# Performance work log

Measured on AMD Instinct MI355X. Metric: run time of the kernel, lower is better.

Reference implementation:

```python
import jax, jax.numpy as jnp
import numpy as np

K = 3          # per-row / per-col topk, from init kwarg k
THRESHOLD = 0.0


def setup_inputs() -> dict:
    key = jax.random.key(0)
    k1, k2 = jax.random.split(key)
    P, R, S = 512, 256, 256
    matching_score_map = jax.random.normal(k1, (P, R, S), dtype=jnp.float32)
    node_corr_scores = jax.random.uniform(k2, (P,), dtype=jnp.float32)
    ref_knn_masks = jnp.ones((P, R), dtype=bool)
    src_knn_masks = jnp.ones((P, S), dtype=bool)
    return {
        "matching_score_map": matching_score_map,
        "node_corr_scores": node_corr_scores,
        "ref_knn_masks": ref_knn_masks,
        "src_knn_masks": src_knn_masks,
    }


def reference(matching_score_map, node_corr_scores, ref_knn_masks, src_knn_masks):
    # score map: exp of log-matching scores  [P, R, S]
    score = jnp.exp(matching_score_map)
    P, R, S = score.shape
    # valid correspondence mask  [P, R, S]
    corr_mask = ref_knn_masks[:, :, None] & src_knn_masks[:, None, :]

    p_idx = jnp.arange(P)[:, None, None]

    # topk along src axis (dim=2), scatter back into a zero map
    ref_vals, ref_idx = jax.lax.top_k(score, K)                      # [P, R, K]
    ref_score_map = jnp.zeros_like(score).at[
        p_idx, jnp.arange(R)[None, :, None], ref_idx
    ].set(ref_vals)

    # topk along ref axis (dim=1): transpose so it is the last axis
    src_vals, src_idx = jax.lax.top_k(score.transpose(0, 2, 1), K)   # [P, S, K]
    src_score_map = jnp.zeros_like(score).at[
        p_idx, src_idx, jnp.arange(S)[None, :, None]
    ].set(src_vals)

    ref_corr_map = (ref_score_map > THRESHOLD) & corr_mask
    src_corr_map = (src_score_map > THRESHOLD) & corr_mask

    score_map = (ref_score_map + src_score_map) * 0.5
    # mutual=False -> logical_or; conditional=False -> no node_corr_scores scaling
    corr_map = ref_corr_map | src_corr_map
    return score_map, corr_map
```

## Files before the change

### kernel.cpp

```cpp
#include <hip/hip_runtime.h>
#include <math.h>
#include <stdint.h>

#define Pn 512
#define Rn 256
#define Sn 256

typedef unsigned long long u64;
typedef unsigned int u32;

__device__ __forceinline__ u32 mono(float f) {
  u32 u = __float_as_uint(f);
  return (u & 0x80000000u) ? ~u : (u | 0x80000000u);
}
__device__ __forceinline__ float unmono(u32 m) {
  u32 bits = (m & 0x80000000u) ? (m & 0x7FFFFFFFu) : ~m;
  return __uint_as_float(bits);
}
__device__ __forceinline__ u64 makekey(float v, int idx) {
  return ((u64)mono(v) << 32) | (u32)(~(u32)idx);
}
__device__ __forceinline__ int key_idx(u64 k) { return (int)(~(u32)k); }
__device__ __forceinline__ float key_val(u64 k) { return unmono((u32)(k >> 32)); }

__device__ __forceinline__ void ins3f(float v, int i,
    float& t0, int& i0, float& t1, int& i1, float& t2, int& i2) {
  const bool b0 = v > t0, b1 = v > t1, b2 = v > t2;
  const float nt0 = b0 ? v : t0;
  const int   ni0 = b0 ? i : i0;
  const float nt1 = b0 ? t0 : (b1 ? v : t1);
  const int   ni1 = b0 ? i0 : (b1 ? i : i1);
  const float nt2 = b1 ? t1 : (b2 ? v : t2);
  const int   ni2 = b1 ? i1 : (b2 ? i : i2);
  t0 = nt0; i0 = ni0; t1 = nt1; i1 = ni1; t2 = nt2; i2 = ni2;
}

__device__ __forceinline__ void ins3k(u64 k, u64& k0, u64& k1, u64& k2) {
  const bool b0 = k > k0, b1 = k > k1, b2 = k > k2;
  const u64 n0 = b0 ? k : k0;
  const u64 n1 = b0 ? k0 : (b1 ? k : k1);
  const u64 n2 = b1 ? k1 : (b2 ? k : k2);
  k0 = n0; k1 = n1; k2 = n2;
}

#define CHUNK 32
#define TSTRIDE 257

__global__ __launch_bounds__(256) void tops_kernel(
    const float* __restrict__ score,
    float* __restrict__ colv, int* __restrict__ coli,
    u64* __restrict__ rowk) {
  __shared__ float tile[CHUNK * TSTRIDE];
  __shared__ u64   pk[8 * CHUNK * 3];
  const int p  = blockIdx.x;
  const int s  = threadIdx.x;
  const int rr = threadIdx.x & 31;
  const int q  = threadIdx.x >> 5;
  const float* base = score + (size_t)p * (Rn * Sn) + s;

  float t0 = -INFINITY, t1 = -INFINITY, t2 = -INFINITY;
  int   i0 = -1, i1 = -1, i2 = -1;

  for (int c = 0; c < 8; ++c) {
    const int r0 = c * CHUNK;
    #pragma unroll 16
    for (int r = 0; r < CHUNK; ++r) {
      const float v = base[(size_t)(r0 + r) * Sn];
      tile[r * TSTRIDE + s] = v;
      ins3f(v, r0 + r, t0, i0, t1, i1, t2, i2);
    }
    __syncthreads();
    u64 k0 = 0, k1 = 0, k2 = 0;
    const int cb = q * 32;
    #pragma unroll 8
    for (int j = 0; j < 32; ++j)
      ins3k(makekey(tile[rr * TSTRIDE + cb + j], cb + j), k0, k1, k2);
    pk[(q * CHUNK + rr) * 3 + 0] = k0;
    pk[(q * CHUNK + rr) * 3 + 1] = k1;
    pk[(q * CHUNK + rr) * 3 + 2] = k2;
    __syncthreads();
    if (threadIdx.x < 32) {
      u64 m0 = pk[threadIdx.x * 3 + 0];
      u64 m1 = pk[threadIdx.x * 3 + 1];
      u64 m2 = pk[threadIdx.x * 3 + 2];
      #pragma unroll
      for (int qq = 1; qq < 8; ++qq) {
        #pragma unroll
        for (int kk = 0; kk < 3; ++kk)
          ins3k(pk[(qq * CHUNK + threadIdx.x) * 3 + kk], m0, m1, m2);
      }
      const size_t ro = ((size_t)p * Rn + r0 + threadIdx.x) * 3;
      rowk[ro + 0] = m0; rowk[ro + 1] = m1; rowk[ro + 2] = m2;
    }
    __syncthreads();
  }
  const size_t PS = (size_t)Pn * Sn;
  const size_t o  = (size_t)p * Sn + s;
  colv[0 * PS + o] = t0; coli[0 * PS + o] = i0;
  colv[1 * PS + o] = t1; coli[1 * PS + o] = i1;
  colv[2 * PS + o] = t2; coli[2 * PS + o] = i2;
}

__device__ __forceinline__ void compute_elem(
    int s, int r, bool rmask, int sm,
    float rv0, float rv1, float rv2, int ri0, int ri1, int ri2,
    float a0, int b0, float a1, int b1, float a2, int b2,
    float& oscore, float& ocorr) {
  const float rv = (s == ri0) ? rv0 : (s == ri1) ? rv1 : (s == ri2) ? rv2 : 0.0f;
  const float sv = (r == b0) ? a0 : (r == b1) ? a1 : (r == b2) ? a2 : 0.0f;
  oscore = 0.5f * (rv + sv);
  const bool m = rmask && (sm != 0);
  ocorr = (((rv > 0.0f) || (sv > 0.0f)) && m) ? 1.0f : 0.0f;
}

__global__ __launch_bounds__(256) void write_kernel(
    const float* __restrict__ colv, const int* __restrict__ coli,
    const u64* __restrict__ rowk,
    const int* __restrict__ rmaskp, const int* __restrict__ smaskp,
    float* __restrict__ out) {
  const int p     = blockIdx.x >> 2;
  const int rbase = (blockIdx.x & 3) * 64;
  const int warp  = threadIdx.x >> 6;
  const int lane  = threadIdx.x & 63;
  const size_t PS = (size_t)Pn * Sn;
  const size_t N  = (size_t)Pn * Rn * Sn;
  const size_t cb = (size_t)p * Sn;

  float4 T0 = reinterpret_cast<const float4*>(colv + 0 * PS + cb)[lane];
  float4 T1 = reinterpret_cast<const float4*>(colv + 1 * PS + cb)[lane];
  float4 T2 = reinterpret_cast<const float4*>(colv + 2 * PS + cb)[lane];
  int4   I0 = reinterpret_cast<const int4*>(coli + 0 * PS + cb)[lane];
  int4   I1 = reinterpret_cast<const int4*>(coli + 1 * PS + cb)[lane];
  int4   I2 = reinterpret_cast<const int4*>(coli + 2 * PS + cb)[lane];
  T0.x = expf(T0.x); T0.y = expf(T0.y); T0.z = expf(T0.z); T0.w = expf(T0.w);
  T1.x = expf(T1.x); T1.y = expf(T1.y); T1.z = expf(T1.z); T1.w = expf(T1.w);
  T2.x = expf(T2.x); T2.y = expf(T2.y); T2.z = expf(T2.z); T2.w = expf(T2.w);

  const int4 sm = reinterpret_cast<const int4*>(smaskp + cb)[lane];
  const int sbase = lane * 4;
  float* outp = out + (size_t)p * (Rn * Sn);

  #pragma unroll 4
  for (int it = 0; it < 16; ++it) {
    const int r = rbase + it * 4 + warp;
    const size_t ro = ((size_t)p * Rn + r) * 3;
    const u64 rk0 = rowk[ro + 0];
    const u64 rk1 = rowk[ro + 1];
    const u64 rk2 = rowk[ro + 2];
    const float rv0 = expf(key_val(rk0));
    const float rv1 = expf(key_val(rk1));
    const float rv2 = expf(key_val(rk2));
    const int   ri0 = key_idx(rk0), ri1 = key_idx(rk1), ri2 = key_idx(rk2);
    const bool  rm  = rmaskp[p * Rn + r] != 0;

    float4 osc, oco;
    compute_elem(sbase + 0, r, rm, sm.x, rv0, rv1, rv2, ri0, ri1, ri2,
                 T0.x, I0.x, T1.x, I1.x, T2.x, I2.x, osc.x, oco.x);
    compute_elem(sbase + 1, r, rm, sm.y, rv0, rv1, rv2, ri0, ri1, ri2,
                 T0.y, I0.y, T1.y, I1.y, T2.y, I2.y, osc.y, oco.y);
    compute_elem(sbase + 2, r, rm, sm.z, rv0, rv1, rv2, ri0, ri1, ri2,
                 T0.z, I0.z, T1.z, I1.z, T2.z, I2.z, osc.z, oco.z);
    compute_elem(sbase + 3, r, rm, sm.w, rv0, rv1, rv2, ri0, ri1, ri2,
                 T0.w, I0.w, T1.w, I1.w, T2.w, I2.w, osc.w, oco.w);

    reinterpret_cast<float4*>(outp + (size_t)r * Sn)[lane]     = osc;
    reinterpret_cast<float4*>(outp + N + (size_t)r * Sn)[lane] = oco;
  }
}

extern "C" void kernel_launch(void* const* d_in, const int* in_sizes, int n_in,
                              void* d_out, int out_size, void* d_ws, size_t ws_size,
                              hipStream_t stream) {
  const float* score = (const float*)d_in[0];
  const int* rmask = (const int*)d_in[2];
  const int* smask = (const int*)d_in[3];
  float* out = (float*)d_out;

  const size_t PS = (size_t)Pn * Sn;
  float* colv = (float*)d_ws;
  int*   coli = (int*)(colv + 3 * PS);
  u64*   rowk = (u64*)(coli + 3 * PS);

  tops_kernel<<<Pn, 256, 0, stream>>>(score, colv, coli, rowk);
  write_kernel<<<Pn * 4, 256, 0, stream>>>(colv, coli, rowk,
                                           rmask, smask, out);
}
```

Before: 394.1 us.

## Fuse top-k and output write kernels into one per-plane kernel

Merges the top-k kernel and the write kernel into one kernel that keeps the per-row and per-column top-3 values and indices in shared memory. The output is then written directly from the same block. This removes the workspace round trip and one launch. In exchange the write phase runs with only 512 blocks instead of 2048, which lowers parallelism for the store-bound part, and shared memory use per block grows.

```diff
diff --git a/kernel.cpp b/kernel.cpp
--- a/kernel.cpp
+++ b/kernel.cpp
@@ -43,20 +43,40 @@
   k0 = n0; k1 = n1; k2 = n2;
 }
 
+__device__ __forceinline__ void compute_elem(
+    int s, int r, bool rmask, int sm,
+    float rv0, float rv1, float rv2, int ri0, int ri1, int ri2,
+    float a0, int b0, float a1, int b1, float a2, int b2,
+    float& oscore, float& ocorr) {
+  const float rv = (s == ri0) ? rv0 : (s == ri1) ? rv1 : (s == ri2) ? rv2 : 0.0f;
+  const float sv = (r == b0) ? a0 : (r == b1) ? a1 : (r == b2) ? a2 : 0.0f;
+  oscore = 0.5f * (rv + sv);
+  const bool m = rmask && (sm != 0);
+  ocorr = (((rv > 0.0f) || (sv > 0.0f)) && m) ? 1.0f : 0.0f;
+}
+
 #define CHUNK 32
 #define TSTRIDE 257
 
-__global__ __launch_bounds__(256) void tops_kernel(
+__global__ __launch_bounds__(256) void fused_kernel(
     const float* __restrict__ score,
-    float* __restrict__ colv, int* __restrict__ coli,
-    u64* __restrict__ rowk) {
+    const int* __restrict__ rmaskp, const int* __restrict__ smaskp,
+    float* __restrict__ out) {
   __shared__ float tile[CHUNK * TSTRIDE];
   __shared__ u64   pk[8 * CHUNK * 3];
+  __shared__ float rowv[Rn * 3];
+  __shared__ int   rowi[Rn * 3];
+  __shared__ float colvs[Sn * 3];
+  __shared__ int   colis[Sn * 3];
+  __shared__ int   rmk[Rn];
+
   const int p  = blockIdx.x;
   const int s  = threadIdx.x;
   const int rr = threadIdx.x & 31;
   const int q  = threadIdx.x >> 5;
   const float* base = score + (size_t)p * (Rn * Sn) + s;
+
+  rmk[s] = rmaskp[p * Rn + s];
 
   float t0 = -INFINITY, t1 = -INFINITY, t2 = -INFINITY;
   int   i0 = -1, i1 = -1, i2 = -1;
@@ -89,79 +109,58 @@
         for (int kk = 0; kk < 3; ++kk)
           ins3k(pk[(qq * CHUNK + threadIdx.x) * 3 + kk], m0, m1, m2);
       }
-      const size_t ro = ((size_t)p * Rn + r0 + threadIdx.x) * 3;
-      rowk[ro + 0] = m0; rowk[ro + 1] = m1; rowk[ro + 2] = m2;
+      const int r = r0 + threadIdx.x;
+      rowv[r * 3 + 0] = expf(key_val(m0)); rowi[r * 3 + 0] = key_idx(m0);
+      rowv[r * 3 + 1] = expf(key_val(m1)); rowi[r * 3 + 1] = key_idx(m1);
+      rowv[r * 3 + 2] = expf(key_val(m2)); rowi[r * 3 + 2] = key_idx(m2);
     }
     __syncthreads();
   }
-  const size_t PS = (size_t)Pn * Sn;
-  const size_t o  = (size_t)p * Sn + s;
-  colv[0 * PS + o] = t0; coli[0 * PS + o] = i0;
-  colv[1 * PS + o] = t1; coli[1 * PS + o] = i1;
-  colv[2 * PS + o] = t2; coli[2 * PS + o] = i2;
-}
 
-__device__ __forceinline__ void compute_elem(
-    int s, int r, bool rmask, int sm,
-    float rv0, float rv1, float rv2, int ri0, int ri1, int ri2,
-    float a0, int b0, float a1, int b1, float a2, int b2,
-    float& oscore, float& ocorr) {
-  const float rv = (s == ri0) ? rv0 : (s == ri1) ? rv1 : (s == ri2) ? rv2 : 0.0f;
-  const float sv = (r == b0) ? a0 : (r == b1) ? a1 : (r == b2) ? a2 : 0.0f;
-  oscore = 0.5f * (rv + sv);
-  const bool m = rmask && (sm != 0);
-  ocorr = (((rv > 0.0f) || (sv > 0.0f)) && m) ? 1.0f : 0.0f;
-}
+  colvs[s * 3 + 0] = expf(t0); colis[s * 3 + 0] = i0;
+  colvs[s * 3 + 1] = expf(t1); colis[s * 3 + 1] = i1;
+  colvs[s * 3 + 2] = expf(t2); colis[s * 3 + 2] = i2;
+  __syncthreads();
 
-__global__ __launch_bounds__(256) void write_kernel(
-    const float* __restrict__ colv, const int* __restrict__ coli,
-    const u64* __restrict__ rowk,
-    const int* __restrict__ rmaskp, const int* __restrict__ smaskp,
-    float* __restrict__ out) {
-  const int p     = blockIdx.x >> 2;
-  const int rbase = (blockIdx.x & 3) * 64;
   const int warp  = threadIdx.x >> 6;
   const int lane  = threadIdx.x & 63;
-  const size_t PS = (size_t)Pn * Sn;
+  const int sbase = lane * 4;
   const size_t N  = (size_t)Pn * Rn * Sn;
-  const size_t cb = (size_t)p * Sn;
-
-  float4 T0 = reinterpret_cast<const float4*>(colv + 0 * PS + cb)[lane];
-  float4 T1 = reinterpret_cast<const float4*>(colv + 1 * PS + cb)[lane];
-  float4 T2 = reinterpret_cast<const float4*>(colv + 2 * PS + cb)[lane];
-  int4   I0 = reinterpret_cast<const int4*>(coli + 0 * PS + cb)[lane];
-  int4   I1 = reinterpret_cast<const int4*>(coli + 1 * PS + cb)[lane];
-  int4   I2 = reinterpret_cast<const int4*>(coli + 2 * PS + cb)[lane];
-  T0.x = expf(T0.x); T0.y = expf(T0.y); T0.z = expf(T0.z); T0.w = expf(T0.w);
-  T1.x = expf(T1.x); T1.y = expf(T1.y); T1.z = expf(T1.z); T1.w = expf(T1.w);
-  T2.x = expf(T2.x); T2.y = expf(T2.y); T2.z = expf(T2.z); T2.w = expf(T2.w);
-
-  const int4 sm = reinterpret_cast<const int4*>(smaskp + cb)[lane];
-  const int sbase = lane * 4;
   float* outp = out + (size_t)p * (Rn * Sn);
 
+  const int4 sm = reinterpret_cast<const int4*>(smaskp + (size_t)p * Sn)[lane];
+
+  float A0x, A0y, A0z, A0w, A1x, A1y, A1z, A1w, A2x, A2y, A2z, A2w;
+  int   B0x, B0y, B0z, B0w, B1x, B1y, B1z, B1w, B2x, B2y, B2z, B2w;
+  A0x = colvs[(sbase + 0) * 3 + 0]; B0x = colis[(sbase + 0) * 3 + 0];
+  A1x = colvs[(sbase + 0) * 3 + 1]; B1x = colis[(sbase + 0) * 3 + 1];
+  A2x = colvs[(sbase + 0) * 3 + 2]; B2x = colis[(sbase + 0) * 3 + 2];
+  A0y = colvs[(sbase + 1) * 3 + 0]; B0y = colis[(sbase + 1) * 3 + 0];
+  A1y = colvs[(sbase + 1) * 3 + 1]; B1y = colis[(sbase + 1) * 3 + 1];
+  A2y = colvs[(sbase + 1) * 3 + 2]; B2y = colis[(sbase + 1) * 3 + 2];
+  A0z = colvs[(sbase + 2) * 3 + 0]; B0z = colis[(sbase + 2) * 3 + 0];
+  A1z = colvs[(sbase + 2) * 3 + 1]; B1z = colis[(sbase + 2) * 3 + 1];
+  A2z = colvs[(sbase + 2) * 3 + 2]; B2z = colis[(sbase + 2) * 3 + 2];
+  A0w = colvs[(sbase + 3) * 3 + 0]; B0w = colis[(sbase + 3) * 3 + 0];
+  A1w = colvs[(sbase + 3) * 3 + 1]; B1w = colis[(sbase + 3) * 3 + 1];
+  A2w = colvs[(sbase + 3) * 3 + 2]; B2w = colis[(sbase + 3) * 3 + 2];
+
   #pragma unroll 4
-  for (int it = 0; it < 16; ++it) {
-    const int r = rbase + it * 4 + warp;
-    const size_t ro = ((size_t)p * Rn + r) * 3;
-    const u64 rk0 = rowk[ro + 0];
-    const u64 rk1 = rowk[ro + 1];
-    const u64 rk2 = rowk[ro + 2];
-    const float rv0 = expf(key_val(rk0));
-    const float rv1 = expf(key_val(rk1));
-    const float rv2 = expf(key_val(rk2));
-    const int   ri0 = key_idx(rk0), ri1 = key_idx(rk1), ri2 = key_idx(rk2);
-    const bool  rm  = rmaskp[p * Rn + r] != 0;
+  for (int it = 0; it < 64; ++it) {
+    const int r = it * 4 + warp;
+    const float rv0 = rowv[r * 3 + 0], rv1 = rowv[r * 3 + 1], rv2 = rowv[r * 3 + 2];
+    const int   ri0 = rowi[r * 3 + 0], ri1 = rowi[r * 3 + 1], ri2 = rowi[r * 3 + 2];
+    const bool  rm  = rmk[r] != 0;
 
     float4 osc, oco;
     compute_elem(sbase + 0, r, rm, sm.x, rv0, rv1, rv2, ri0, ri1, ri2,
-                 T0.x, I0.x, T1.x, I1.x, T2.x, I2.x, osc.x, oco.x);
+                 A0x, B0x, A1x, B1x, A2x, B2x, osc.x, oco.x);
     compute_elem(sbase + 1, r, rm, sm.y, rv0, rv1, rv2, ri0, ri1, ri2,
-                 T0.y, I0.y, T1.y, I1.y, T2.y, I2.y, osc.y, oco.y);
+                 A0y, B0y, A1y, B1y, A2y, B2y, osc.y, oco.y);
     compute_elem(sbase + 2, r, rm, sm.z, rv0, rv1, rv2, ri0, ri1, ri2,
-                 T0.z, I0.z, T1.z, I1.z, T2.z, I2.z, osc.z, oco.z);
+                 A0z, B0z, A1z, B1z, A2z, B2z, osc.z, oco.z);
     compute_elem(sbase + 3, r, rm, sm.w, rv0, rv1, rv2, ri0, ri1, ri2,
-                 T0.w, I0.w, T1.w, I1.w, T2.w, I2.w, osc.w, oco.w);
+                 A0w, B0w, A1w, B1w, A2w, B2w, osc.w, oco.w);
 
     reinterpret_cast<float4*>(outp + (size_t)r * Sn)[lane]     = osc;
     reinterpret_cast<float4*>(outp + N + (size_t)r * Sn)[lane] = oco;
@@ -175,13 +174,7 @@
   const int* rmask = (const int*)d_in[2];
   const int* smask = (const int*)d_in[3];
   float* out = (float*)d_out;
+  (void)d_ws; (void)ws_size;
 
-  const size_t PS = (size_t)Pn * Sn;
-  float* colv = (float*)d_ws;
-  int*   coli = (int*)(colv + 3 * PS);
-  u64*   rowk = (u64*)(coli + 3 * PS);
-
-  tops_kernel<<<Pn, 256, 0, stream>>>(score, colv, coli, rowk);
-  write_kernel<<<Pn * 4, 256, 0, stream>>>(colv, coli, rowk,
-                                           rmask, smask, out);
+  fused_kernel<<<Pn, 256, 0, stream>>>(score, rmask, smask, out);
 }
```

New measurement: 416.0 us. +5.6%, slower.

## Split top-k pass into two row-halves per plane and merge column partials later

Applied to the files above, without the earlier changes.

The top-k kernel now launches two blocks per plane, each scanning half the rows, so more blocks run concurrently on the GPU. Column partial top-3 lists are written per half and merged in the write kernel. Row top-k uses float/int pairs instead of packed 64-bit keys and exponentiates once in the first kernel. The write kernel stages row values and masks in shared memory. The cost is extra workspace traffic for the doubled column partials and a merge step in the write kernel. Ties are now broken by strict greater-than rather than by packed key order.

```diff
diff --git a/kernel.cpp b/kernel.cpp
--- a/kernel.cpp
+++ b/kernel.cpp
@@ -6,22 +6,8 @@
 #define Rn 256
 #define Sn 256
 
-typedef unsigned long long u64;
-typedef unsigned int u32;
-
-__device__ __forceinline__ u32 mono(float f) {
-  u32 u = __float_as_uint(f);
-  return (u & 0x80000000u) ? ~u : (u | 0x80000000u);
-}
-__device__ __forceinline__ float unmono(u32 m) {
-  u32 bits = (m & 0x80000000u) ? (m & 0x7FFFFFFFu) : ~m;
-  return __uint_as_float(bits);
-}
-__device__ __forceinline__ u64 makekey(float v, int idx) {
-  return ((u64)mono(v) << 32) | (u32)(~(u32)idx);
-}
-__device__ __forceinline__ int key_idx(u64 k) { return (int)(~(u32)k); }
-__device__ __forceinline__ float key_val(u64 k) { return unmono((u32)(k >> 32)); }
+#define CHUNK 32
+#define TSTRIDE 257
 
 __device__ __forceinline__ void ins3f(float v, int i,
     float& t0, int& i0, float& t1, int& i1, float& t2, int& i2) {
@@ -35,70 +21,68 @@
   t0 = nt0; i0 = ni0; t1 = nt1; i1 = ni1; t2 = nt2; i2 = ni2;
 }
 
-__device__ __forceinline__ void ins3k(u64 k, u64& k0, u64& k1, u64& k2) {
-  const bool b0 = k > k0, b1 = k > k1, b2 = k > k2;
-  const u64 n0 = b0 ? k : k0;
-  const u64 n1 = b0 ? k0 : (b1 ? k : k1);
-  const u64 n2 = b1 ? k1 : (b2 ? k : k2);
-  k0 = n0; k1 = n1; k2 = n2;
-}
-
-#define CHUNK 32
-#define TSTRIDE 257
-
-__global__ __launch_bounds__(256) void tops_kernel(
+__global__ __launch_bounds__(256, 4) void tops_kernel(
     const float* __restrict__ score,
-    float* __restrict__ colv, int* __restrict__ coli,
-    u64* __restrict__ rowk) {
+    float* __restrict__ colpv, int* __restrict__ colpi,
+    float* __restrict__ rowvg, int* __restrict__ rowig) {
   __shared__ float tile[CHUNK * TSTRIDE];
-  __shared__ u64   pk[8 * CHUNK * 3];
-  const int p  = blockIdx.x;
+  __shared__ float pv[8 * CHUNK * 3];
+  __shared__ int   pi[8 * CHUNK * 3];
+  const int p  = blockIdx.x >> 1;
+  const int h  = blockIdx.x & 1;
   const int s  = threadIdx.x;
   const int rr = threadIdx.x & 31;
   const int q  = threadIdx.x >> 5;
-  const float* base = score + (size_t)p * (Rn * Sn) + s;
+  const int rowbase = h * 128;
+  const float* base = score + (size_t)p * (Rn * Sn) + (size_t)rowbase * Sn + s;
 
   float t0 = -INFINITY, t1 = -INFINITY, t2 = -INFINITY;
   int   i0 = -1, i1 = -1, i2 = -1;
 
-  for (int c = 0; c < 8; ++c) {
+  for (int c = 0; c < 4; ++c) {
     const int r0 = c * CHUNK;
-    #pragma unroll 16
+    #pragma unroll
     for (int r = 0; r < CHUNK; ++r) {
       const float v = base[(size_t)(r0 + r) * Sn];
       tile[r * TSTRIDE + s] = v;
-      ins3f(v, r0 + r, t0, i0, t1, i1, t2, i2);
+      ins3f(v, rowbase + r0 + r, t0, i0, t1, i1, t2, i2);
     }
     __syncthreads();
-    u64 k0 = 0, k1 = 0, k2 = 0;
+    float k0 = -INFINITY, k1 = -INFINITY, k2 = -INFINITY;
+    int   j0 = -1, j1 = -1, j2 = -1;
     const int cb = q * 32;
-    #pragma unroll 8
+    #pragma unroll
     for (int j = 0; j < 32; ++j)
-      ins3k(makekey(tile[rr * TSTRIDE + cb + j], cb + j), k0, k1, k2);
-    pk[(q * CHUNK + rr) * 3 + 0] = k0;
-    pk[(q * CHUNK + rr) * 3 + 1] = k1;
-    pk[(q * CHUNK + rr) * 3 + 2] = k2;
+      ins3f(tile[rr * TSTRIDE + cb + j], cb + j, k0, j0, k1, j1, k2, j2);
+    const int pb = (q * CHUNK + rr) * 3;
+    pv[pb + 0] = k0; pi[pb + 0] = j0;
+    pv[pb + 1] = k1; pi[pb + 1] = j1;
+    pv[pb + 2] = k2; pi[pb + 2] = j2;
     __syncthreads();
     if (threadIdx.x < 32) {
-      u64 m0 = pk[threadIdx.x * 3 + 0];
-      u64 m1 = pk[threadIdx.x * 3 + 1];
-      u64 m2 = pk[threadIdx.x * 3 + 2];
+      float m0 = pv[threadIdx.x * 3 + 0], m1 = pv[threadIdx.x * 3 + 1],
+            m2 = pv[threadIdx.x * 3 + 2];
+      int   n0 = pi[threadIdx.x * 3 + 0], n1 = pi[threadIdx.x * 3 + 1],
+            n2 = pi[threadIdx.x * 3 + 2];
       #pragma unroll
       for (int qq = 1; qq < 8; ++qq) {
+        const int b = (qq * CHUNK + threadIdx.x) * 3;
         #pragma unroll
         for (int kk = 0; kk < 3; ++kk)
-          ins3k(pk[(qq * CHUNK + threadIdx.x) * 3 + kk], m0, m1, m2);
+          ins3f(pv[b + kk], pi[b + kk], m0, n0, m1, n1, m2, n2);
       }
-      const size_t ro = ((size_t)p * Rn + r0 + threadIdx.x) * 3;
-      rowk[ro + 0] = m0; rowk[ro + 1] = m1; rowk[ro + 2] = m2;
+      const size_t ro = ((size_t)p * Rn + rowbase + r0 + threadIdx.x) * 3;
+      rowvg[ro + 0] = expf(m0); rowig[ro + 0] = n0;
+      rowvg[ro + 1] = expf(m1); rowig[ro + 1] = n1;
+      rowvg[ro + 2] = expf(m2); rowig[ro + 2] = n2;
     }
     __syncthreads();
   }
   const size_t PS = (size_t)Pn * Sn;
   const size_t o  = (size_t)p * Sn + s;
-  colv[0 * PS + o] = t0; coli[0 * PS + o] = i0;
-  colv[1 * PS + o] = t1; coli[1 * PS + o] = i1;
-  colv[2 * PS + o] = t2; coli[2 * PS + o] = i2;
+  colpv[(h * 3 + 0) * PS + o] = t0; colpi[(h * 3 + 0) * PS + o] = i0;
+  colpv[(h * 3 + 1) * PS + o] = t1; colpi[(h * 3 + 1) * PS + o] = i1;
+  colpv[(h * 3 + 2) * PS + o] = t2; colpi[(h * 3 + 2) * PS + o] = i2;
 }
 
 __device__ __forceinline__ void compute_elem(
@@ -114,24 +98,44 @@
 }
 
 __global__ __launch_bounds__(256) void write_kernel(
-    const float* __restrict__ colv, const int* __restrict__ coli,
-    const u64* __restrict__ rowk,
+    const float* __restrict__ colpv, const int* __restrict__ colpi,
+    const float* __restrict__ rowvg, const int* __restrict__ rowig,
     const int* __restrict__ rmaskp, const int* __restrict__ smaskp,
     float* __restrict__ out) {
+  __shared__ float rv[64 * 3];
+  __shared__ int   ri[64 * 3];
+  __shared__ int   rmk[64];
   const int p     = blockIdx.x >> 2;
   const int rbase = (blockIdx.x & 3) * 64;
-  const int warp  = threadIdx.x >> 6;
-  const int lane  = threadIdx.x & 63;
+  const int tid   = threadIdx.x;
+  if (tid < 192) {
+    const size_t rb = ((size_t)p * Rn + rbase) * 3;
+    rv[tid] = rowvg[rb + tid];
+    ri[tid] = rowig[rb + tid];
+  }
+  if (tid < 64) rmk[tid] = rmaskp[p * Rn + rbase + tid];
+
+  const int warp  = tid >> 6;
+  const int lane  = tid & 63;
   const size_t PS = (size_t)Pn * Sn;
   const size_t N  = (size_t)Pn * Rn * Sn;
   const size_t cb = (size_t)p * Sn;
 
-  float4 T0 = reinterpret_cast<const float4*>(colv + 0 * PS + cb)[lane];
-  float4 T1 = reinterpret_cast<const float4*>(colv + 1 * PS + cb)[lane];
-  float4 T2 = reinterpret_cast<const float4*>(colv + 2 * PS + cb)[lane];
-  int4   I0 = reinterpret_cast<const int4*>(coli + 0 * PS + cb)[lane];
-  int4   I1 = reinterpret_cast<const int4*>(coli + 1 * PS + cb)[lane];
-  int4   I2 = reinterpret_cast<const int4*>(coli + 2 * PS + cb)[lane];
+  float4 T0 = reinterpret_cast<const float4*>(colpv + 0 * PS + cb)[lane];
+  float4 T1 = reinterpret_cast<const float4*>(colpv + 1 * PS + cb)[lane];
+  float4 T2 = reinterpret_cast<const float4*>(colpv + 2 * PS + cb)[lane];
+  int4   I0 = reinterpret_cast<const int4*>(colpi + 0 * PS + cb)[lane];
+  int4   I1 = reinterpret_cast<const int4*>(colpi + 1 * PS + cb)[lane];
+  int4   I2 = reinterpret_cast<const int4*>(colpi + 2 * PS + cb)[lane];
+  #pragma unroll
+  for (int k = 3; k < 6; ++k) {
+    const float4 V = reinterpret_cast<const float4*>(colpv + (size_t)k * PS + cb)[lane];
+    const int4   J = reinterpret_cast<const int4*>(colpi + (size_t)k * PS + cb)[lane];
+    ins3f(V.x, J.x, T0.x, I0.x, T1.x, I1.x, T2.x, I2.x);
+    ins3f(V.y, J.y, T0.y, I0.y, T1.y, I1.y, T2.y, I2.y);
+    ins3f(V.z, J.z, T0.z, I0.z, T1.z, I1.z, T2.z, I2.z);
+    ins3f(V.w, J.w, T0.w, I0.w, T1.w, I1.w, T2.w, I2.w);
+  }
   T0.x = expf(T0.x); T0.y = expf(T0.y); T0.z = expf(T0.z); T0.w = expf(T0.w);
   T1.x = expf(T1.x); T1.y = expf(T1.y); T1.z = expf(T1.z); T1.w = expf(T1.w);
   T2.x = expf(T2.x); T2.y = expf(T2.y); T2.z = expf(T2.z); T2.w = expf(T2.w);
@@ -139,19 +143,15 @@
   const int4 sm = reinterpret_cast<const int4*>(smaskp + cb)[lane];
   const int sbase = lane * 4;
   float* outp = out + (size_t)p * (Rn * Sn);
+  __syncthreads();
 
   #pragma unroll 4
   for (int it = 0; it < 16; ++it) {
-    const int r = rbase + it * 4 + warp;
-    const size_t ro = ((size_t)p * Rn + r) * 3;
-    const u64 rk0 = rowk[ro + 0];
-    const u64 rk1 = rowk[ro + 1];
-    const u64 rk2 = rowk[ro + 2];
-    const float rv0 = expf(key_val(rk0));
-    const float rv1 = expf(key_val(rk1));
-    const float rv2 = expf(key_val(rk2));
-    const int   ri0 = key_idx(rk0), ri1 = key_idx(rk1), ri2 = key_idx(rk2);
-    const bool  rm  = rmaskp[p * Rn + r] != 0;
+    const int rl = it * 4 + warp;
+    const int r  = rbase + rl;
+    const float rv0 = rv[rl * 3 + 0], rv1 = rv[rl * 3 + 1], rv2 = rv[rl * 3 + 2];
+    const int   ri0 = ri[rl * 3 + 0], ri1 = ri[rl * 3 + 1], ri2 = ri[rl * 3 + 2];
+    const bool  rm  = rmk[rl] != 0;
 
     float4 osc, oco;
     compute_elem(sbase + 0, r, rm, sm.x, rv0, rv1, rv2, ri0, ri1, ri2,
@@ -177,11 +177,12 @@
   float* out = (float*)d_out;
 
   const size_t PS = (size_t)Pn * Sn;
-  float* colv = (float*)d_ws;
-  int*   coli = (int*)(colv + 3 * PS);
-  u64*   rowk = (u64*)(coli + 3 * PS);
+  float* colpv = (float*)d_ws;
+  int*   colpi = (int*)(colpv + 6 * PS);
+  float* rowvg = (float*)(colpi + 6 * PS);
+  int*   rowig = (int*)(rowvg + (size_t)Pn * Rn * 3);
 
-  tops_kernel<<<Pn, 256, 0, stream>>>(score, colv, coli, rowk);
-  write_kernel<<<Pn * 4, 256, 0, stream>>>(colv, coli, rowk,
+  tops_kernel<<<Pn * 2, 256, 0, stream>>>(score, colpv, colpi, rowvg, rowig);
+  write_kernel<<<Pn * 4, 256, 0, stream>>>(colpv, colpi, rowvg, rowig,
                                            rmask, smask, out);
 }
```

New measurement: 444.6 us. 12.8% more time.
